# Optimization experiments

Hardware: AMD Instinct MI355X
Metric: run time of the kernel (lower is better)

The kernel has to match this reference:

```python
import jax, jax.numpy as jnp
import numpy as np
from jax import lax

BOS = 0
B, T, U = 8, 256, 64
IN, ENC_H, DEC_H, P, J, V = 80, 512, 512, 512, 512, 1024


def lstm_layer(x, Wih, Whh, b):
    """PyTorch-style LSTM layer. x: [B,T,I]; Wih: [4H,I]; Whh: [4H,H]; b: [4H]."""
    Bn = x.shape[0]
    H = Whh.shape[1]
    xp = jnp.einsum('bti,gi->btg', x, Wih) + b  # precompute input projections [B,T,4H]
    h0 = jnp.zeros((Bn, H), x.dtype)

    def step(carry, xt):
        h, c = carry
        g = xt + h @ Whh.T
        i, f, gg, o = jnp.split(g, 4, axis=-1)
        c = jax.nn.sigmoid(f) * c + jax.nn.sigmoid(i) * jnp.tanh(gg)
        h = jax.nn.sigmoid(o) * jnp.tanh(c)
        return (h, c), h

    _, hs = lax.scan(step, (h0, h0), xp.transpose(1, 0, 2))
    return hs.transpose(1, 0, 2)  # [B,T,H]


def setup_inputs() -> dict:
    key = jax.random.key(0)
    ks = jax.random.split(key, 20)
    s = 0.04  # ~1/sqrt(H) init scale
    inp = {
        'xs': jax.random.normal(ks[0], (B, T, IN), jnp.float32),
        'ys': jax.random.randint(ks[1], (B, U), 0, V),
        # encoder LSTM layer 0 / 1
        'enc_Wih0': jax.random.normal(ks[2], (4 * ENC_H, IN), jnp.float32) * s,
        'enc_Whh0': jax.random.normal(ks[3], (4 * ENC_H, ENC_H), jnp.float32) * s,
        'enc_b0': jnp.zeros((4 * ENC_H,), jnp.float32),
        'enc_Wih1': jax.random.normal(ks[4], (4 * ENC_H, ENC_H), jnp.float32) * s,
        'enc_Whh1': jax.random.normal(ks[5], (4 * ENC_H, ENC_H), jnp.float32) * s,
        'enc_b1': jnp.zeros((4 * ENC_H,), jnp.float32),
        'enc_projW': jax.random.normal(ks[6], (P, ENC_H), jnp.float32) * s,
        'enc_projb': jnp.zeros((P,), jnp.float32),
        # decoder
        'embed': jax.random.normal(ks[7], (V, DEC_H), jnp.float32) * s,
        'dec_Wih': jax.random.normal(ks[8], (4 * DEC_H, DEC_H), jnp.float32) * s,
        'dec_Whh': jax.random.normal(ks[9], (4 * DEC_H, DEC_H), jnp.float32) * s,
        'dec_b': jnp.zeros((4 * DEC_H,), jnp.float32),
        'dec_projW': jax.random.normal(ks[10], (P, DEC_H), jnp.float32) * s,
        'dec_projb': jnp.zeros((P,), jnp.float32),
        # joint MLP: Linear(2P -> J), Tanh, Linear(J -> V)
        'jW1': jax.random.normal(ks[11], (J, 2 * P), jnp.float32) * s,
        'jb1': jnp.zeros((J,), jnp.float32),
        'jW2': jax.random.normal(ks[12], (V, J), jnp.float32) * s,
        'jb2': jnp.zeros((V,), jnp.float32),
    }
    return inp


def reference(xs, ys, enc_Wih0, enc_Whh0, enc_b0, enc_Wih1, enc_Whh1, enc_b1,
              enc_projW, enc_projb, embed, dec_Wih, dec_Whh, dec_b,
              dec_projW, dec_projb, jW1, jb1, jW2, jb2):
    # Encoder: 2-layer LSTM + projection
    h = lstm_layer(xs, enc_Wih0, enc_Whh0, enc_b0)
    h = lstm_layer(h, enc_Wih1, enc_Whh1, enc_b1)
    h_enc = h @ enc_projW.T + enc_projb  # [B,T,P]

    # Decoder: BOS pad, embed, 1-layer LSTM + projection
    ys_p = jnp.pad(ys, ((0, 0), (1, 0)), constant_values=BOS)  # [B,U+1]
    e = embed[ys_p]
    hd = lstm_layer(e, dec_Wih, dec_Whh, dec_b)
    h_dec = hd @ dec_projW.T + dec_projb  # [B,U+1,P]

    # Joint: cat([h_enc,h_dec]) @ W1.T == h_enc @ W1[:,:P].T + h_dec @ W1[:,P:].T
    pre_enc = jnp.einsum('btp,jp->btj', h_enc, jW1[:, :P])
    pre_dec = jnp.einsum('bup,jp->buj', h_dec, jW1[:, P:])
    z = jnp.tanh(pre_enc[:, :, None, :] + pre_dec[:, None, :, :] + jb1)  # [B,T,U+1,J]
    logits = jnp.einsum('btuj,vj->btuv', z, jW2) + jb2  # [B,T,U+1,V]
    return logits
```

## Files before the change

kernel.cpp:

```cpp
#include <hip/hip_runtime.h>


typedef _Float16 f16;
typedef _Float16 f16x8 __attribute__((ext_vector_type(8)));
typedef float f32x4 __attribute__((ext_vector_type(4)));
using u32 = unsigned int;

#define BB   8
#define TT   256
#define UU1  65
#define HH   512
#define G4   2048
#define PP   512
#define JJ   512
#define VV   1024
#define SENT 0xFFFFFFFFu

#define LOADX(p)     __hip_atomic_load((p), __ATOMIC_RELAXED, __HIP_MEMORY_SCOPE_AGENT)
#define STOREX(p, v) __hip_atomic_store((p), (v), __ATOMIC_RELAXED, __HIP_MEMORY_SCOPE_AGENT)

static __device__ __forceinline__ u32 packf16(float a, float b) {
  f16 ha = (f16)a, hb = (f16)b;
  unsigned short ua = __builtin_bit_cast(unsigned short, ha);
  unsigned short ub = __builtin_bit_cast(unsigned short, hb);
  return (u32)ua | ((u32)ub << 16);
}
static __device__ __forceinline__ float sigm(float x) {
  x = fminf(30.f, fmaxf(-30.f, x));
  return __builtin_amdgcn_rcpf(1.f + __expf(-x));
}
static __device__ __forceinline__ float ftanh(float x) {
  x = fminf(15.f, fmaxf(-15.f, x));
  float t = __expf(2.f * x);
  return (t - 1.f) * __builtin_amdgcn_rcpf(t + 1.f);
}

__global__ void k_zero(u32* __restrict__ p, int n) {
  int i = blockIdx.x * 256 + threadIdx.x;
  if (i < n) p[i] = 0u;
}
__global__ void k_fill(u32* __restrict__ p, int n, u32 v) {
  int i = blockIdx.x * 256 + threadIdx.x;
  if (i < n) p[i] = v;
}

struct CastSeg { const float* s; f16* d; int n4; };
struct CastArgs { CastSeg seg[10]; };
__global__ void k_cast_all(CastArgs a, int total4) {
  int i = blockIdx.x * 256 + threadIdx.x;
  if (i >= total4) return;
  int k = 0, off = i;
  while (off >= a.seg[k].n4) { off -= a.seg[k].n4; ++k; }
  const float4 v = *(const float4*)(a.seg[k].s + (size_t)off * 4);
  uint2 p; p.x = packf16(v.x, v.y); p.y = packf16(v.z, v.w);
  *(uint2*)(a.seg[k].d + (size_t)off * 4) = p;
}

__global__ void k_embed(const int* __restrict__ ys, const float* __restrict__ emb,
                        float* __restrict__ e) {
  int row = blockIdx.x;
  int b = row / UU1, u = row % UU1;
  int idx = (u == 0) ? 0 : ys[b * (UU1 - 1) + (u - 1)];
  const float4* s = (const float4*)(emb + (size_t)idx * HH);
  float4* d = (float4*)(e + (size_t)row * HH);
  d[threadIdx.x] = s[threadIdx.x];
}

__global__ __launch_bounds__(256) void k_gemm(
    const float* __restrict__ A, const f16* __restrict__ B,
    const float* __restrict__ bias, float* __restrict__ C,
    int M, int N, int K, int lda, int ldb) {
  __shared__ f16 As[128][72];
  __shared__ f16 Bs[128][72];
  int tid = threadIdx.x;
  int mb = blockIdx.y * 128, nb = blockIdx.x * 128;
  int wave = tid >> 6, lane = tid & 63;
  int wm = wave >> 1, wn = wave & 1;
  int rowa = lane & 15, kg = lane >> 4;
  f32x4 acc[4][4] = {};
  for (int k0 = 0; k0 < K; k0 += 64) {
    for (int idx = tid; idx < 2048; idx += 256) {
      int r = idx >> 4, cq = idx & 15;
      int gm = mb + r, gk = k0 + cq * 4;
      float4 v = make_float4(0.f, 0.f, 0.f, 0.f);
      if (gm < M && gk + 3 < K) v = *(const float4*)(A + (size_t)gm * lda + gk);
      uint2 p; p.x = packf16(v.x, v.y); p.y = packf16(v.z, v.w);
      *(uint2*)&As[r][cq * 4] = p;
    }
    for (int idx = tid; idx < 1024; idx += 256) {
      int r = idx >> 3, c8 = idx & 7;
      int gn = nb + r, gk = k0 + c8 * 8;
      uint4 v = make_uint4(0u, 0u, 0u, 0u);
      if (gn < N && gk + 7 < K) v = *(const uint4*)(B + (size_t)gn * ldb + gk);
      *(uint4*)&Bs[r][c8 * 8] = v;
    }
    __syncthreads();
#pragma unroll
    for (int kf = 0; kf < 2; ++kf) {
      f16x8 af[4], bf[4];
#pragma unroll
      for (int mt = 0; mt < 4; ++mt)
        af[mt] = *(const f16x8*)&As[wm * 64 + mt * 16 + rowa][kf * 32 + kg * 8];
#pragma unroll
      for (int nt = 0; nt < 4; ++nt)
        bf[nt] = *(const f16x8*)&Bs[wn * 64 + nt * 16 + rowa][kf * 32 + kg * 8];
#pragma unroll
      for (int mt = 0; mt < 4; ++mt)
#pragma unroll
        for (int nt = 0; nt < 4; ++nt)
          acc[mt][nt] = __builtin_amdgcn_mfma_f32_16x16x32_f16(af[mt], bf[nt], acc[mt][nt], 0, 0, 0);
    }
    __syncthreads();
  }
#pragma unroll
  for (int nt = 0; nt < 4; ++nt) {
    int gn = nb + wn * 64 + nt * 16 + rowa;
    float bv = bias ? bias[gn] : 0.f;
#pragma unroll
    for (int mt = 0; mt < 4; ++mt)
#pragma unroll
      for (int r = 0; r < 4; ++r) {
        int gm = mb + wm * 64 + mt * 16 + kg * 4 + r;
        if (gm < M) C[(size_t)gm * N + gn] = acc[mt][nt][r] + bv;
      }
  }
}

template <int NW>
static __device__ __forceinline__ void poll_batch(const u32* const* p, u32* vv) {
#pragma unroll
  for (int k = 0; k < NW; ++k) vv[k] = LOADX(p[k]);
  int gd = 0;
  while (++gd < (1 << 18)) {
    bool any = false;
#pragma unroll
    for (int k = 0; k < NW; ++k) any = any | (vv[k] == SENT);
    if (!any) break;
    __builtin_amdgcn_s_sleep(4);
#pragma unroll
    for (int k = 0; k < NW; ++k)
      if (vv[k] == SENT) vv[k] = LOADX(p[k]);
  }
}
static __device__ __forceinline__ void guard_spin(const u32* gp) {
  u32 v = LOADX(gp);
  int gd = 0;
  while (v == SENT && ++gd < (1 << 18)) {
    __builtin_amdgcn_s_sleep(2);
    v = LOADX(gp);
  }
}

static __device__ __forceinline__ void lstm_16(
    int wg, const float* __restrict__ xp, const f16* __restrict__ Whh,
    u32* __restrict__ hseq,
    float* __restrict__ hs, int S) {
  extern __shared__ char smem[];
  f16 (*W)[520] = (f16(*)[520])smem;
  f16 (*H)[520] = (f16(*)[520])(smem + 133120);
  float (*gat)[132] = (float(*)[132])(smem + 133120 + 8320);
  const int tid = threadIdx.x;
  const int u0 = wg * 32;
  const int wave = tid >> 6, lane = tid & 63;
  const int rowa = lane & 15, kg = lane >> 4;
  const int b = tid >> 5, j = tid & 31;

  for (int idx = tid; idx < 128 * 64; idx += 256) {
    int r = idx >> 6, ck = idx & 63;
    int g = r >> 5, i = r & 31;
    uint4 v = *(const uint4*)(Whh + ((size_t)(g * 512 + u0 + i)) * 512 + ck * 8);
    *(uint4*)&W[r][ck * 8] = v;
  }
  __syncthreads();

  float c = 0.f;
  for (int t = 0; t < S; ++t) {
    size_t xpo = ((size_t)b * S + t) * (size_t)G4 + u0 + j;
    float xi = xp[xpo], xf = xp[xpo + 512], xg = xp[xpo + 1024], xo = xp[xpo + 1536];

    const u32* hb = hseq + (size_t)t * 2048;
    if (tid < 16) guard_spin(hb + tid * 16);
    __syncthreads();
    const u32* ptr[8];
    u32 vv[8];
#pragma unroll
    for (int k = 0; k < 8; ++k) ptr[k] = hb + ((tid + k * 256) >> 8) * 256 + ((tid + k * 256) & 255);
    poll_batch<8>(ptr, vv);
#pragma unroll
    for (int k = 0; k < 8; ++k) {
      int idx = tid + k * 256;
      ((u32*)H)[(idx >> 8) * 260 + (idx & 255)] = vv[k];
    }
    __syncthreads();

    f32x4 acc0 = {0.f, 0.f, 0.f, 0.f}, acc1 = {0.f, 0.f, 0.f, 0.f};
#pragma unroll
    for (int kf = 0; kf < 16; ++kf) {
      f16x8 af = {};
      if (rowa < 8) af = *(const f16x8*)&H[rowa][kf * 32 + kg * 8];
      f16x8 b0 = *(const f16x8*)&W[wave * 32 + rowa][kf * 32 + kg * 8];
      f16x8 b1 = *(const f16x8*)&W[wave * 32 + 16 + rowa][kf * 32 + kg * 8];
      acc0 = __builtin_amdgcn_mfma_f32_16x16x32_f16(af, b0, acc0, 0, 0, 0);
      acc1 = __builtin_amdgcn_mfma_f32_16x16x32_f16(af, b1, acc1, 0, 0, 0);
    }
    if (kg < 2) {
#pragma unroll
      for (int r = 0; r < 4; ++r) {
        gat[kg * 4 + r][wave * 32 + rowa] = acc0[r];
        gat[kg * 4 + r][wave * 32 + 16 + rowa] = acc1[r];
      }
    }
    __syncthreads();

    float gi = gat[b][j] + xi;
    float gf = gat[b][32 + j] + xf;
    float gg = gat[b][64 + j] + xg;
    float go = gat[b][96 + j] + xo;
    c = sigm(gf) * c + sigm(gi) * ftanh(gg);
    float h = sigm(go) * ftanh(c);

    float hn = __shfl_down(h, 1);
    if ((j & 1) == 0)
      STOREX(hseq + (size_t)(t + 1) * 2048 + ((b * 512 + u0 + j) >> 1), packf16(h, hn));
    if (hs) hs[((size_t)b * S + t) * HH + u0 + j] = h;
  }
}

static __device__ __forceinline__ void lstm_l1(
    int wg, const float* __restrict__ gb, const f16* __restrict__ Wih,
    const f16* __restrict__ Whh, const u32* __restrict__ hin,
    u32* __restrict__ hseq, float* __restrict__ hs, int S) {
  extern __shared__ char smem[];
  f16 (*W)[1032] = (f16(*)[1032])smem;
  f16 (*H)[1032] = (f16(*)[1032])(smem + 132096);
  float (*gat)[68] = (float(*)[68])(smem + 132096 + 16512);
  const int tid = threadIdx.x;
  const int u0 = wg * 16;
  const int wave = tid >> 6, lane = tid & 63;
  const int rowa = lane & 15, kg = lane >> 4;

  for (int idx = tid; idx < 64 * 64; idx += 256) {
    int r = idx >> 6, ck = idx & 63;
    int g = r >> 4, i = r & 15;
    size_t grow = (size_t)(g * 512 + u0 + i) * 512;
    *(uint4*)&W[r][ck * 8]       = *(const uint4*)(Whh + grow + ck * 8);
    *(uint4*)&W[r][512 + ck * 8] = *(const uint4*)(Wih + grow + ck * 8);
  }
  float gbi = 0.f, gbf = 0.f, gbg = 0.f, gbo = 0.f;
  if (tid < 128) {
    int jj = tid & 15;
    gbi = gb[u0 + jj]; gbf = gb[512 + u0 + jj];
    gbg = gb[1024 + u0 + jj]; gbo = gb[1536 + u0 + jj];
  }
  __syncthreads();

  float c = 0.f;
  for (int t = 0; t < S; ++t) {
    const u32* hbS = hseq + (size_t)t * 2048;
    const u32* hbU = hin + (size_t)(t + 1) * 2048;
    if (tid < 32)       guard_spin(hbS + tid * 8);
    else if (tid < 48)  guard_spin(hbU + (tid - 32) * 16);
    __syncthreads();
    const u32* ptr[16];
    u32 vv[16];
#pragma unroll
    for (int k = 0; k < 8; ++k) {
      int idx = tid + k * 256;
      int r = idx >> 8, cu = idx & 255;
      ptr[k] = hbS + r * 256 + cu;
      ptr[k + 8] = hbU + r * 256 + cu;
    }
    poll_batch<16>(ptr, vv);
#pragma unroll
    for (int k = 0; k < 8; ++k) {
      int idx = tid + k * 256;
      int r = idx >> 8, cu = idx & 255;
      ((u32*)H)[r * 516 + cu] = vv[k];
      ((u32*)H)[r * 516 + 256 + cu] = vv[k + 8];
    }
    __syncthreads();

    f32x4 accA = {0.f, 0.f, 0.f, 0.f}, accB = {0.f, 0.f, 0.f, 0.f};
#pragma unroll
    for (int kf = 0; kf < 16; ++kf) {
      f16x8 afA = {}, afB = {};
      if (rowa < 8) {
        afA = *(const f16x8*)&H[rowa][kf * 32 + kg * 8];
        afB = *(const f16x8*)&H[rowa][(kf + 16) * 32 + kg * 8];
      }
      f16x8 bfA = *(const f16x8*)&W[wave * 16 + rowa][kf * 32 + kg * 8];
      f16x8 bfB = *(const f16x8*)&W[wave * 16 + rowa][(kf + 16) * 32 + kg * 8];
      accA = __builtin_amdgcn_mfma_f32_16x16x32_f16(afA, bfA, accA, 0, 0, 0);
      accB = __builtin_amdgcn_mfma_f32_16x16x32_f16(afB, bfB, accB, 0, 0, 0);
    }
    if (kg < 2) {
#pragma unroll
      for (int r = 0; r < 4; ++r) gat[kg * 4 + r][wave * 16 + rowa] = accA[r] + accB[r];
    }
    __syncthreads();

    if (tid < 128) {
      int b = tid >> 4, j = tid & 15;
      float gi = gat[b][j]      + gbi;
      float gf = gat[b][16 + j] + gbf;
      float gg = gat[b][32 + j] + gbg;
      float go = gat[b][48 + j] + gbo;
      c = sigm(gf) * c + sigm(gi) * ftanh(gg);
      float h = sigm(go) * ftanh(c);
      float hn = __shfl_down(h, 1);
      if ((j & 1) == 0)
        STOREX(hseq + (size_t)(t + 1) * 2048 + (b * 256 + ((u0 + j) >> 1)), packf16(h, hn));
      hs[((size_t)b * S + t) * HH + u0 + j] = h;
    }
  }
}

__global__ __launch_bounds__(256, 1) void k_lstm3(
    const float* xp0, const f16* Whh0, u32* hseq0,
    const float* b1, const f16* Wih1, const f16* Whh1, u32* hseq1, float* h1s,
    const float* xpd, const f16* Whhd, u32* hseqD, float* hds) {
  int g = blockIdx.x;
  if (g < 16)      lstm_16(g, xp0, Whh0, hseq0, nullptr, TT);
  else if (g < 48) lstm_l1(g - 16, b1, Wih1, Whh1, hseq0, hseq1, h1s, TT);
  else             lstm_16(g - 48, xpd, Whhd, hseqD, hds, UU1);
}

__global__ __launch_bounds__(512) void k_joint(
    const float* __restrict__ pre_enc,
    const float* __restrict__ pre_dec,
    const f16* __restrict__ jW2,
    const float* __restrict__ jb2,
    float* __restrict__ out) {
  extern __shared__ char smem[];
  f16 (*Z)[520] = (f16(*)[520])smem;
  int tid = threadIdx.x;
  int m0 = blockIdx.x * 64;
  {
    int r = tid >> 3, q = tid & 7;
    int m = m0 + r;
    int bb = m / (TT * UU1);
    int rem = m % (TT * UU1);
    int t = rem / UU1, u = rem % UU1;
    const float* pe = pre_enc + ((size_t)bb * TT + t) * JJ + q * 64;
    const float* pd = pre_dec + ((size_t)bb * UU1 + u) * JJ + q * 64;
    for (int i = 0; i < 64; i += 8) {
      float4 e0 = *(const float4*)(pe + i);
      float4 e1 = *(const float4*)(pe + i + 4);
      float4 d0 = *(const float4*)(pd + i);
      float4 d1 = *(const float4*)(pd + i + 4);
      float z0 = ftanh(e0.x + d0.x), z1 = ftanh(e0.y + d0.y);
      float z2 = ftanh(e0.z + d0.z), z3 = ftanh(e0.w + d0.w);
      float z4 = ftanh(e1.x + d1.x), z5 = ftanh(e1.y + d1.y);
      float z6 = ftanh(e1.z + d1.z), z7 = ftanh(e1.w + d1.w);
      uint4 p; p.x = packf16(z0, z1); p.y = packf16(z2, z3);
      p.z = packf16(z4, z5); p.w = packf16(z6, z7);
      *(uint4*)&Z[r][q * 64 + i] = p;
    }
  }
  __syncthreads();
  int wave = tid >> 6, lane = tid & 63;
  int wm = wave >> 2, wn = wave & 3;
  int rowa = lane & 15, kg = lane >> 4;
  for (int ch = 0; ch < 4; ++ch) {
    f32x4 acc[2][4] = {};
    int nb = ch * 256 + wn * 64;
    for (int kf = 0; kf < 16; ++kf) {
      f16x8 af[2], bf[4];
#pragma unroll
      for (int mt = 0; mt < 2; ++mt)
        af[mt] = *(const f16x8*)&Z[wm * 32 + mt * 16 + rowa][kf * 32 + kg * 8];
#pragma unroll
      for (int nt = 0; nt < 4; ++nt)
        bf[nt] = *(const f16x8*)(jW2 + (size_t)(nb + nt * 16 + rowa) * JJ + kf * 32 + kg * 8);
#pragma unroll
      for (int mt = 0; mt < 2; ++mt)
#pragma unroll
        for (int nt = 0; nt < 4; ++nt)
          acc[mt][nt] = __builtin_amdgcn_mfma_f32_16x16x32_f16(af[mt], bf[nt], acc[mt][nt], 0, 0, 0);
    }
#pragma unroll
    for (int nt = 0; nt < 4; ++nt) {
      int v = nb + nt * 16 + rowa;
      float bv = jb2[v];
#pragma unroll
      for (int mt = 0; mt < 2; ++mt)
#pragma unroll
        for (int r = 0; r < 4; ++r) {
          int m = m0 + wm * 32 + mt * 16 + kg * 4 + r;
          out[(size_t)m * VV + v] = acc[mt][nt][r] + bv;
        }
    }
  }
}

extern "C" void kernel_launch(void* const* d_in, const int* in_sizes, int n_in,
                              void* d_out, int out_size, void* d_ws, size_t ws_size,
                              hipStream_t stream) {
  const float* xs    = (const float*)d_in[0];
  const int*   ys    = (const int*)d_in[1];
  const float* Wih0  = (const float*)d_in[2];
  const float* Whh0  = (const float*)d_in[3];
  const float* b0    = (const float*)d_in[4];
  const float* Wih1  = (const float*)d_in[5];
  const float* Whh1  = (const float*)d_in[6];
  const float* b1    = (const float*)d_in[7];
  const float* encPW = (const float*)d_in[8];
  const float* encPb = (const float*)d_in[9];
  const float* embed = (const float*)d_in[10];
  const float* dWih  = (const float*)d_in[11];
  const float* dWhh  = (const float*)d_in[12];
  const float* db    = (const float*)d_in[13];
  const float* dPW   = (const float*)d_in[14];
  const float* dPb   = (const float*)d_in[15];
  const float* jW1   = (const float*)d_in[16];
  const float* jb1   = (const float*)d_in[17];
  const float* jW2   = (const float*)d_in[18];
  const float* jb2   = (const float*)d_in[19];
  float* out = (float*)d_out;

  char* base = (char*)d_ws;
  size_t off = 0;
  auto alc = [&](size_t bytes) -> char* {
    char* p = base + off;
    off = (off + bytes + 255) & ~(size_t)255;
    return p;
  };
  f16* Wih0h = (f16*)alc((size_t)2048 * 80 * 2);
  f16* Whh0h = (f16*)alc((size_t)2048 * 512 * 2);
  f16* Wih1h = (f16*)alc((size_t)2048 * 512 * 2);
  f16* Whh1h = (f16*)alc((size_t)2048 * 512 * 2);
  f16* dWihh = (f16*)alc((size_t)2048 * 512 * 2);
  f16* dWhhh = (f16*)alc((size_t)2048 * 512 * 2);
  f16* ePWh  = (f16*)alc((size_t)512 * 512 * 2);
  f16* dPWh  = (f16*)alc((size_t)512 * 512 * 2);
  f16* jW1h  = (f16*)alc((size_t)512 * 1024 * 2);
  f16* jW2h  = (f16*)alc((size_t)1024 * 512 * 2);
  float* e    = (float*)alc((size_t)520 * 512 * 4);
  float* xp0  = (float*)alc((size_t)2048 * 2048 * 4);
  float* xpd  = (float*)alc((size_t)520 * 2048 * 4);
  float* h1s  = (float*)alc((size_t)2048 * 512 * 4);
  float* hds  = (float*)alc((size_t)520 * 512 * 4);
  float* henc = (float*)alc((size_t)2048 * 512 * 4);
  float* hdec = (float*)alc((size_t)520 * 512 * 4);
  float* penc = (float*)alc((size_t)2048 * 512 * 4);
  float* pdec = (float*)alc((size_t)520 * 512 * 4);
  u32* hseq0 = (u32*)alc((size_t)(TT + 1) * 2048 * 4);
  u32* hseq1 = (u32*)alc((size_t)(TT + 1) * 2048 * 4);
  u32* hseqD = (u32*)alc((size_t)(UU1 + 1) * 2048 * 4);
  if (off > ws_size) return;

  {
    int n = (int)(((TT + 1) * 2 + (UU1 + 1)) * 2048);
    k_fill<<<dim3((n + 255) / 256), dim3(256), 0, stream>>>(hseq0, n, SENT);
    k_zero<<<dim3(8), dim3(256), 0, stream>>>(hseq0, 2048);
    k_zero<<<dim3(8), dim3(256), 0, stream>>>(hseq1, 2048);
    k_zero<<<dim3(8), dim3(256), 0, stream>>>(hseqD, 2048);
  }
  {
    CastArgs ca;
    auto seg = [&](int i, const float* s, f16* d, size_t n) {
      ca.seg[i].s = s; ca.seg[i].d = d; ca.seg[i].n4 = (int)(n / 4);
    };
    seg(0, Wih0, Wih0h, (size_t)2048 * 80);
    seg(1, Whh0, Whh0h, (size_t)2048 * 512);
    seg(2, Wih1, Wih1h, (size_t)2048 * 512);
    seg(3, Whh1, Whh1h, (size_t)2048 * 512);
    seg(4, dWih, dWihh, (size_t)2048 * 512);
    seg(5, dWhh, dWhhh, (size_t)2048 * 512);
    seg(6, encPW, ePWh, (size_t)512 * 512);
    seg(7, dPW, dPWh, (size_t)512 * 512);
    seg(8, jW1, jW1h, (size_t)512 * 1024);
    seg(9, jW2, jW2h, (size_t)1024 * 512);
    int total4 = 0;
    for (int i = 0; i < 10; ++i) total4 += ca.seg[i].n4;
    k_cast_all<<<dim3((total4 + 255) / 256), dim3(256), 0, stream>>>(ca, total4);
  }

  k_embed<<<dim3(520), dim3(128), 0, stream>>>(ys, embed, e);

  auto gemm = [&](const float* A, const f16* B, const float* bias, float* C,
                  int M, int N, int K, int lda, int ldb) {
    k_gemm<<<dim3(N / 128, (M + 127) / 128), dim3(256), 0, stream>>>(
        A, B, bias, C, M, N, K, lda, ldb);
  };

  gemm(xs, Wih0h, b0, xp0, 2048, 2048, 80, 80, 80);
  gemm(e, dWihh, db, xpd, 520, 2048, 512, 512, 512);

  k_lstm3<<<dim3(64), dim3(256), 150784, stream>>>(
      xp0, Whh0h, hseq0,
      b1, Wih1h, Whh1h, hseq1, h1s,
      xpd, dWhhh, hseqD, hds);

  gemm(h1s, ePWh, encPb, henc, 2048, 512, 512, 512, 512);
  gemm(henc, jW1h, nullptr, penc, 2048, 512, 512, 512, 1024);
  gemm(hds, dPWh, dPb, hdec, 520, 512, 512, 512, 512);
  gemm(hdec, jW1h + 512, jb1, pdec, 520, 512, 512, 512, 1024);

  k_joint<<<dim3(2080), dim3(512), 66560, stream>>>(penc, pdec, jW2h, jb2, out);
}
```

Measured before the change: 1.618 ms.

## Make LSTM gate combine wave-local, transpose joint output stores, fuse init kernels

Reorders Whh rows in LDS so that each wave holds all four gates for its own subset of hidden units. The gate nonlinearity can then read only its own wave's accumulators, which drops one block-wide __syncthreads per recurrent step in both LSTM variants. The joint kernel swaps MFMA operand roles so each lane holds four consecutive vocab outputs, writing them as float4 nontemporal stores with a vector bias load. The four sentinel/zero init launches are merged into one kernel. The wave-local gate read relies on same-wave LDS ordering without a barrier, and the transposed operands change the register layout of the accumulators.

After: 1.589 ms. No clear change (-1.8%).

```diff
diff --git a/kernel.cpp b/kernel.cpp
--- a/kernel.cpp
+++ b/kernel.cpp
@@ -35,13 +35,11 @@
   return (t - 1.f) * __builtin_amdgcn_rcpf(t + 1.f);
 }
 
-__global__ void k_zero(u32* __restrict__ p, int n) {
+__global__ void k_init(u32* __restrict__ p, int n, int z1, int z2) {
   int i = blockIdx.x * 256 + threadIdx.x;
-  if (i < n) p[i] = 0u;
-}
-__global__ void k_fill(u32* __restrict__ p, int n, u32 v) {
-  int i = blockIdx.x * 256 + threadIdx.x;
-  if (i < n) p[i] = v;
+  if (i >= n) return;
+  bool z = (i < 2048) | ((u32)(i - z1) < 2048u) | ((u32)(i - z2) < 2048u);
+  p[i] = z ? 0u : SENT;
 }
 
 struct CastSeg { const float* s; f16* d; int n4; };
@@ -158,29 +156,31 @@
   extern __shared__ char smem[];
   f16 (*W)[520] = (f16(*)[520])smem;
   f16 (*H)[520] = (f16(*)[520])(smem + 133120);
-  float (*gat)[132] = (float(*)[132])(smem + 133120 + 8320);
+  float (*gat)[8][36] = (float(*)[8][36])(smem + 133120 + 8320);
   const int tid = threadIdx.x;
   const int u0 = wg * 32;
   const int wave = tid >> 6, lane = tid & 63;
   const int rowa = lane & 15, kg = lane >> 4;
-  const int b = tid >> 5, j = tid & 31;
+  const int b = lane >> 3, ju = lane & 7;
+  const int uglob = u0 + wave * 8 + ju;
 
   for (int idx = tid; idx < 128 * 64; idx += 256) {
     int r = idx >> 6, ck = idx & 63;
-    int g = r >> 5, i = r & 31;
-    uint4 v = *(const uint4*)(Whh + ((size_t)(g * 512 + u0 + i)) * 512 + ck * 8);
+    int w = r >> 5, g = (r >> 3) & 3, u = r & 7;
+    uint4 v = *(const uint4*)(Whh + ((size_t)(g * 512 + u0 + w * 8 + u)) * 512 + ck * 8);
     *(uint4*)&W[r][ck * 8] = v;
   }
   __syncthreads();
 
   float c = 0.f;
   for (int t = 0; t < S; ++t) {
-    size_t xpo = ((size_t)b * S + t) * (size_t)G4 + u0 + j;
-    float xi = xp[xpo], xf = xp[xpo + 512], xg = xp[xpo + 1024], xo = xp[xpo + 1536];
-
     const u32* hb = hseq + (size_t)t * 2048;
     if (tid < 16) guard_spin(hb + tid * 16);
     __syncthreads();
+
+    size_t xpo = ((size_t)b * S + t) * (size_t)G4 + uglob;
+    float xi = xp[xpo], xf = xp[xpo + 512], xg = xp[xpo + 1024], xo = xp[xpo + 1536];
+
     const u32* ptr[8];
     u32 vv[8];
 #pragma unroll
@@ -206,23 +206,21 @@
     if (kg < 2) {
 #pragma unroll
       for (int r = 0; r < 4; ++r) {
-        gat[kg * 4 + r][wave * 32 + rowa] = acc0[r];
-        gat[kg * 4 + r][wave * 32 + 16 + rowa] = acc1[r];
+        gat[wave][kg * 4 + r][rowa] = acc0[r];
+        gat[wave][kg * 4 + r][16 + rowa] = acc1[r];
       }
     }
-    __syncthreads();
-
-    float gi = gat[b][j] + xi;
-    float gf = gat[b][32 + j] + xf;
-    float gg = gat[b][64 + j] + xg;
-    float go = gat[b][96 + j] + xo;
+    float gi = gat[wave][b][ju] + xi;
+    float gf = gat[wave][b][8 + ju] + xf;
+    float gg = gat[wave][b][16 + ju] + xg;
+    float go = gat[wave][b][24 + ju] + xo;
     c = sigm(gf) * c + sigm(gi) * ftanh(gg);
     float h = sigm(go) * ftanh(c);
 
     float hn = __shfl_down(h, 1);
-    if ((j & 1) == 0)
-      STOREX(hseq + (size_t)(t + 1) * 2048 + ((b * 512 + u0 + j) >> 1), packf16(h, hn));
-    if (hs) hs[((size_t)b * S + t) * HH + u0 + j] = h;
+    if ((ju & 1) == 0)
+      STOREX(hseq + (size_t)(t + 1) * 2048 + ((b * 512 + uglob) >> 1), packf16(h, hn));
+    if (hs) hs[((size_t)b * S + t) * HH + uglob] = h;
   }
 }
 
@@ -233,24 +231,25 @@
   extern __shared__ char smem[];
   f16 (*W)[1032] = (f16(*)[1032])smem;
   f16 (*H)[1032] = (f16(*)[1032])(smem + 132096);
-  float (*gat)[68] = (float(*)[68])(smem + 132096 + 16512);
+  float (*gat)[8][20] = (float(*)[8][20])(smem + 132096 + 16512);
   const int tid = threadIdx.x;
   const int u0 = wg * 16;
   const int wave = tid >> 6, lane = tid & 63;
   const int rowa = lane & 15, kg = lane >> 4;
+  const int b = lane >> 2, ju = lane & 3;
+  const int uglob = u0 + wave * 4 + ju;
 
   for (int idx = tid; idx < 64 * 64; idx += 256) {
     int r = idx >> 6, ck = idx & 63;
-    int g = r >> 4, i = r & 15;
-    size_t grow = (size_t)(g * 512 + u0 + i) * 512;
+    int w = r >> 4, g = (r >> 2) & 3, u = r & 3;
+    size_t grow = (size_t)(g * 512 + u0 + w * 4 + u) * 512;
     *(uint4*)&W[r][ck * 8]       = *(const uint4*)(Whh + grow + ck * 8);
     *(uint4*)&W[r][512 + ck * 8] = *(const uint4*)(Wih + grow + ck * 8);
   }
   float gbi = 0.f, gbf = 0.f, gbg = 0.f, gbo = 0.f;
-  if (tid < 128) {
-    int jj = tid & 15;
-    gbi = gb[u0 + jj]; gbf = gb[512 + u0 + jj];
-    gbg = gb[1024 + u0 + jj]; gbo = gb[1536 + u0 + jj];
+  if (lane < 32) {
+    gbi = gb[uglob]; gbf = gb[512 + uglob];
+    gbg = gb[1024 + uglob]; gbo = gb[1536 + uglob];
   }
   __syncthreads();
 
@@ -295,22 +294,19 @@
     }
     if (kg < 2) {
 #pragma unroll
-      for (int r = 0; r < 4; ++r) gat[kg * 4 + r][wave * 16 + rowa] = accA[r] + accB[r];
-    }
-    __syncthreads();
-
-    if (tid < 128) {
-      int b = tid >> 4, j = tid & 15;
-      float gi = gat[b][j]      + gbi;
-      float gf = gat[b][16 + j] + gbf;
-      float gg = gat[b][32 + j] + gbg;
-      float go = gat[b][48 + j] + gbo;
+      for (int r = 0; r < 4; ++r) gat[wave][kg * 4 + r][rowa] = accA[r] + accB[r];
+    }
+    if (lane < 32) {
+      float gi = gat[wave][b][ju]      + gbi;
+      float gf = gat[wave][b][4 + ju]  + gbf;
+      float gg = gat[wave][b][8 + ju]  + gbg;
+      float go = gat[wave][b][12 + ju] + gbo;
       c = sigm(gf) * c + sigm(gi) * ftanh(gg);
       float h = sigm(go) * ftanh(c);
       float hn = __shfl_down(h, 1);
-      if ((j & 1) == 0)
-        STOREX(hseq + (size_t)(t + 1) * 2048 + (b * 256 + ((u0 + j) >> 1)), packf16(h, hn));
-      hs[((size_t)b * S + t) * HH + u0 + j] = h;
+      if ((ju & 1) == 0)
+        STOREX(hseq + (size_t)(t + 1) * 2048 + (b * 256 + (uglob >> 1)), packf16(h, hn));
+      hs[((size_t)b * S + t) * HH + uglob] = h;
     }
   }
 }
@@ -362,33 +358,36 @@
   int wm = wave >> 2, wn = wave & 3;
   int rowa = lane & 15, kg = lane >> 4;
   for (int ch = 0; ch < 4; ++ch) {
-    f32x4 acc[2][4] = {};
+    f32x4 acc[4][2] = {};
     int nb = ch * 256 + wn * 64;
     for (int kf = 0; kf < 16; ++kf) {
-      f16x8 af[2], bf[4];
+      f16x8 af[4], bf[2];
+#pragma unroll
+      for (int nt = 0; nt < 4; ++nt)
+        af[nt] = *(const f16x8*)(jW2 + (size_t)(nb + nt * 16 + rowa) * JJ + kf * 32 + kg * 8);
 #pragma unroll
       for (int mt = 0; mt < 2; ++mt)
-        af[mt] = *(const f16x8*)&Z[wm * 32 + mt * 16 + rowa][kf * 32 + kg * 8];
+        bf[mt] = *(const f16x8*)&Z[wm * 32 + mt * 16 + rowa][kf * 32 + kg * 8];
 #pragma unroll
       for (int nt = 0; nt < 4; ++nt)
-        bf[nt] = *(const f16x8*)(jW2 + (size_t)(nb + nt * 16 + rowa) * JJ + kf * 32 + kg * 8);
-#pragma unroll
-      for (int mt = 0; mt < 2; ++mt)
-#pragma unroll
-        for (int nt = 0; nt < 4; ++nt)
-          acc[mt][nt] = __builtin_amdgcn_mfma_f32_16x16x32_f16(af[mt], bf[nt], acc[mt][nt], 0, 0, 0);
+#pragma unroll
+        for (int mt = 0; mt < 2; ++mt)
+          acc[nt][mt] = __builtin_amdgcn_mfma_f32_16x16x32_f16(af[nt], bf[mt], acc[nt][mt], 0, 0, 0);
     }
 #pragma unroll
     for (int nt = 0; nt < 4; ++nt) {
-      int v = nb + nt * 16 + rowa;
-      float bv = jb2[v];
-#pragma unroll
-      for (int mt = 0; mt < 2; ++mt)
-#pragma unroll
-        for (int r = 0; r < 4; ++r) {
-          int m = m0 + wm * 32 + mt * 16 + kg * 4 + r;
-          out[(size_t)m * VV + v] = acc[mt][nt][r] + bv;
-        }
+      int v = nb + nt * 16 + kg * 4;
+      float4 bv = *(const float4*)(jb2 + v);
+#pragma unroll
+      for (int mt = 0; mt < 2; ++mt) {
+        int m = m0 + wm * 32 + mt * 16 + rowa;
+        f32x4 st;
+        st[0] = acc[nt][mt][0] + bv.x;
+        st[1] = acc[nt][mt][1] + bv.y;
+        st[2] = acc[nt][mt][2] + bv.z;
+        st[3] = acc[nt][mt][3] + bv.w;
+        __builtin_nontemporal_store(st, (f32x4*)(out + (size_t)m * VV + v));
+      }
     }
   }
 }
@@ -451,10 +450,8 @@
 
   {
     int n = (int)(((TT + 1) * 2 + (UU1 + 1)) * 2048);
-    k_fill<<<dim3((n + 255) / 256), dim3(256), 0, stream>>>(hseq0, n, SENT);
-    k_zero<<<dim3(8), dim3(256), 0, stream>>>(hseq0, 2048);
-    k_zero<<<dim3(8), dim3(256), 0, stream>>>(hseq1, 2048);
-    k_zero<<<dim3(8), dim3(256), 0, stream>>>(hseqD, 2048);
+    int z1 = (int)(hseq1 - hseq0), z2 = (int)(hseqD - hseq0);
+    k_init<<<dim3((n + 255) / 256), dim3(256), 0, stream>>>(hseq0, n, z1, z2);
   }
   {
     CastArgs ca;
@@ -487,7 +484,7 @@
   gemm(xs, Wih0h, b0, xp0, 2048, 2048, 80, 80, 80);
   gemm(e, dWihh, db, xpd, 520, 2048, 512, 512, 512);
 
-  k_lstm3<<<dim3(64), dim3(256), 150784, stream>>>(
+  k_lstm3<<<dim3(64), dim3(256), 151168, stream>>>(
       xp0, Whh0h, hseq0,
       b1, Wih1h, Whh1h, hseq1, h1s,
       xpd, dWhhh, hseqD, hds);
```
